# Kernel optimization log

Measured on AMD Instinct MI355X. Metric: run time of the kernel, lower is better.

Reference implementation:

```python
import jax, jax.numpy as jnp
import numpy as np

B, M_CONS, F = 32768, 32, 4
N_ITERS = 400  # fixed-iteration projected-gradient on the dual (Q = I so dual is a box-constrained QP)


def setup_inputs() -> dict:
    key = jax.random.key(0)
    kA, kx, kv, ks = jax.random.split(key, 4)
    A = jax.random.normal(kA, (B, M_CONS, F), dtype=jnp.float32)
    x = jax.random.normal(kx, (B, F), dtype=jnp.float32)
    # Construct b so the polyhedron {w : 2 A w <= b} is nonempty (v0 feasible)
    # with small slacks so many constraints are active (nontrivial QP).
    v0 = jax.random.normal(kv, (B, F), dtype=jnp.float32)
    slack = jnp.abs(jax.random.normal(ks, (B, M_CONS), dtype=jnp.float32)) * 0.1
    b = 2.0 * jnp.einsum('bmf,bf->bm', A, v0) + slack
    return {"A": A, "x": x, "b": b}


def reference(A, x, b):
    # Original: min_z 0.5 z^T Q z + p^T z  s.t. G z <= b, with Q = I (2F x 2F),
    #   G = [A | A]  (cat along feature dim), p = -[x; -x] = [-x; x].
    # Dual (Q = I): min_{lam >= 0} lam^T (G G^T) lam / 1 ... f(lam) = lam^T M lam + q^T lam
    #   with M = 0.5 * 2 * G G^T handled below; z* = -(p + G^T lam*).
    f = x.shape[-1]
    G = jnp.concatenate([A, A], axis=2)            # [B, m, 2F]
    p = jnp.concatenate([-x, x], axis=1)           # [B, 2F]
    M = jnp.einsum('bmi,bni->bmn', G, G)           # [B, m, m] = G G^T
    q = jnp.einsum('bmi,bi->bm', G, p) + b         # [B, m]
    # dual objective: 0.5 lam^T M lam + q^T lam, grad = M lam + q, lam >= 0
    # Lipschitz bound for step size: ||M||_2 <= ||M||_F
    L = jnp.sqrt(jnp.sum(M * M, axis=(1, 2))) + 1e-6   # [B]
    alpha = (1.0 / L)[:, None]                     # [B, 1]
    lam0 = jnp.zeros_like(b)

    def step(lam, _):
        grad = jnp.einsum('bmn,bn->bm', M, lam) + q
        lam = jax.nn.relu(lam - alpha * grad)
        return lam, None

    lam, _ = jax.lax.scan(step, lam0, None, length=N_ITERS)
    z = -(p + jnp.einsum('bmi,bm->bi', G, lam))    # [B, 2F]
    # (y[0:F] + y[F:]) / 2
    return (z[:, :f] + z[:, f:]) * 0.5
```

## Files before the change

### kernel.cpp

```cpp
#include <hip/hip_runtime.h>


#define QP_ITERS 400

typedef float v2f __attribute__((ext_vector_type(2)));

template <int CTRL>
__device__ __forceinline__ float dpp_add(float v) {
    return v + __int_as_float(
        __builtin_amdgcn_update_dpp(0, __float_as_int(v), CTRL, 0xF, 0xF, true));
}

__device__ __forceinline__ float quad_sum(float v) {
    v = dpp_add<0xB1>(v);
    v = dpp_add<0x4E>(v);
    return v;
}

__global__ void __launch_bounds__(256)
__attribute__((amdgpu_waves_per_eu(1, 2)))
qp_pgd_kernel(
        const float* __restrict__ A,
        const float* __restrict__ b,
        float* __restrict__ out,
        int nprob) {
    int t = blockIdx.x * blockDim.x + threadIdx.x;
    int p = t >> 2;
    int j = t & 3;
    if (p >= nprob) return;

    const float4* Ar = reinterpret_cast<const float4*>(A + (size_t)p * 128 + (size_t)j * 32);
    const float4* br = reinterpret_cast<const float4*>(b + (size_t)p * 32 + (size_t)j * 8);

    float ax[8], ay[8], az[8], aw[8];
#pragma unroll
    for (int k = 0; k < 8; ++k) {
        float4 r = Ar[k];
        ax[k] = r.x; ay[k] = r.y; az[k] = r.z; aw[k] = r.w;
    }
    float bb[8];
    {
        float4 b0 = br[0], b1 = br[1];
        bb[0] = b0.x; bb[1] = b0.y; bb[2] = b0.z; bb[3] = b0.w;
        bb[4] = b1.x; bb[5] = b1.y; bb[6] = b1.z; bb[7] = b1.w;
    }

    float s00 = 0.f, s01 = 0.f, s02 = 0.f, s03 = 0.f;
    float s11 = 0.f, s12 = 0.f, s13 = 0.f;
    float s22 = 0.f, s23 = 0.f, s33 = 0.f;
#pragma unroll
    for (int k = 0; k < 8; ++k) {
        s00 = fmaf(ax[k], ax[k], s00);
        s01 = fmaf(ax[k], ay[k], s01);
        s02 = fmaf(ax[k], az[k], s02);
        s03 = fmaf(ax[k], aw[k], s03);
        s11 = fmaf(ay[k], ay[k], s11);
        s12 = fmaf(ay[k], az[k], s12);
        s13 = fmaf(ay[k], aw[k], s13);
        s22 = fmaf(az[k], az[k], s22);
        s23 = fmaf(az[k], aw[k], s23);
        s33 = fmaf(aw[k], aw[k], s33);
    }
    s00 = quad_sum(s00); s01 = quad_sum(s01); s02 = quad_sum(s02); s03 = quad_sum(s03);
    s11 = quad_sum(s11); s12 = quad_sum(s12); s13 = quad_sum(s13);
    s22 = quad_sum(s22); s23 = quad_sum(s23); s33 = quad_sum(s33);
    float ssq = s00 * s00 + s11 * s11 + s22 * s22 + s33 * s33
              + 2.f * (s01 * s01 + s02 * s02 + s03 * s03
                     + s12 * s12 + s13 * s13 + s23 * s23);
    float L = 2.f * sqrtf(ssq) + 1e-6f;
    float alpha = 1.f / L;
    float sc = sqrtf(2.f * alpha);
    float inv_sc = 1.f / sc;

    v2f axp[4], ayp[4], azp[4], awp[4], mcp[4], lamp[4];
#pragma unroll
    for (int i = 0; i < 4; ++i) {
        axp[i] = (v2f){ax[2 * i] * sc, ax[2 * i + 1] * sc};
        ayp[i] = (v2f){ay[2 * i] * sc, ay[2 * i + 1] * sc};
        azp[i] = (v2f){az[2 * i] * sc, az[2 * i + 1] * sc};
        awp[i] = (v2f){aw[2 * i] * sc, aw[2 * i + 1] * sc};
        mcp[i] = (v2f){-alpha * bb[2 * i], -alpha * bb[2 * i + 1]};
        lamp[i] = (v2f){0.f, 0.f};
    }

    for (int it = 0; it < QP_ITERS; ++it) {
        v2f a0 = (v2f){0.f, 0.f}, a1 = (v2f){0.f, 0.f};
        v2f a2 = (v2f){0.f, 0.f}, a3 = (v2f){0.f, 0.f};
#pragma unroll
        for (int i = 0; i < 4; ++i) {
            a0 = __builtin_elementwise_fma(axp[i], lamp[i], a0);
            a1 = __builtin_elementwise_fma(ayp[i], lamp[i], a1);
            a2 = __builtin_elementwise_fma(azp[i], lamp[i], a2);
            a3 = __builtin_elementwise_fma(azp[i], lamp[i], a3);
        }
        a3 = (v2f){0.f, 0.f};
#pragma unroll
        for (int i = 0; i < 4; ++i)
            a3 = __builtin_elementwise_fma(awp[i], lamp[i], a3);

        float u0 = a0.x + a0.y, u1 = a1.x + a1.y;
        float u2 = a2.x + a2.y, u3 = a3.x + a3.y;
        u0 = quad_sum(u0); u1 = quad_sum(u1); u2 = quad_sum(u2); u3 = quad_sum(u3);
        v2f U0 = (v2f){-u0, -u0}, U1 = (v2f){-u1, -u1};
        v2f U2 = (v2f){-u2, -u2}, U3 = (v2f){-u3, -u3};
        const v2f z2 = (v2f){0.f, 0.f};
#pragma unroll
        for (int i = 0; i < 4; ++i) {
            v2f tt = lamp[i] + mcp[i];
            tt = __builtin_elementwise_fma(axp[i], U0, tt);
            tt = __builtin_elementwise_fma(ayp[i], U1, tt);
            tt = __builtin_elementwise_fma(azp[i], U2, tt);
            tt = __builtin_elementwise_fma(awp[i], U3, tt);
            lamp[i] = __builtin_elementwise_max(tt, z2);
        }
    }

    v2f a0 = (v2f){0.f, 0.f}, a1 = (v2f){0.f, 0.f};
    v2f a2 = (v2f){0.f, 0.f}, a3 = (v2f){0.f, 0.f};
#pragma unroll
    for (int i = 0; i < 4; ++i) {
        a0 = __builtin_elementwise_fma(axp[i], lamp[i], a0);
        a1 = __builtin_elementwise_fma(ayp[i], lamp[i], a1);
        a2 = __builtin_elementwise_fma(azp[i], lamp[i], a2);
        a3 = __builtin_elementwise_fma(awp[i], lamp[i], a3);
    }
    float u0 = a0.x + a0.y, u1 = a1.x + a1.y;
    float u2 = a2.x + a2.y, u3 = a3.x + a3.y;
    u0 = quad_sum(u0); u1 = quad_sum(u1); u2 = quad_sum(u2); u3 = quad_sum(u3);
    float r = (j & 1) ? ((j & 2) ? u3 : u1) : ((j & 2) ? u2 : u0);
    out[(size_t)p * 4 + j] = -r * inv_sc;
}

extern "C" void kernel_launch(void* const* d_in, const int* in_sizes, int n_in,
                              void* d_out, int out_size, void* d_ws, size_t ws_size,
                              hipStream_t stream) {
    const float* A = (const float*)d_in[0];
    const float* b = (const float*)d_in[2];
    float* out = (float*)d_out;

    int nprob = in_sizes[2] / 32;
    int threads = nprob * 4;
    dim3 block(256);
    dim3 grid((threads + 255) / 256);
    hipLaunchKernelGGL(qp_pgd_kernel, grid, block, 0, stream, A, b, out, nprob);
}
```

Before: 93.23 us.

## Split each QP across two lanes instead of four to cut shuffle reductions

Each problem is now handled by 2 threads with 16 constraints each instead of 4 threads with 8, so the per-iteration cross-lane reduction needs one DPP step instead of two. It also removes the redundant a3 accumulation over azp, unrolls the iteration loop by 2, tightens waves_per_eu to 1, and writes the output as float2. The cost is fewer total threads (half the waves) and double the per-thread registers, which reduces latency hiding and occupancy.

```diff
diff --git a/kernel.cpp b/kernel.cpp
--- a/kernel.cpp
+++ b/kernel.cpp
@@ -11,45 +11,44 @@
         __builtin_amdgcn_update_dpp(0, __float_as_int(v), CTRL, 0xF, 0xF, true));
 }
 
-__device__ __forceinline__ float quad_sum(float v) {
-    v = dpp_add<0xB1>(v);
-    v = dpp_add<0x4E>(v);
-    return v;
+__device__ __forceinline__ float pair_sum(float v) {
+    return dpp_add<0xB1>(v);
 }
 
 __global__ void __launch_bounds__(256)
-__attribute__((amdgpu_waves_per_eu(1, 2)))
+__attribute__((amdgpu_waves_per_eu(1, 1)))
 qp_pgd_kernel(
         const float* __restrict__ A,
         const float* __restrict__ b,
         float* __restrict__ out,
         int nprob) {
     int t = blockIdx.x * blockDim.x + threadIdx.x;
-    int p = t >> 2;
-    int j = t & 3;
+    int p = t >> 1;
+    int j = t & 1;
     if (p >= nprob) return;
 
-    const float4* Ar = reinterpret_cast<const float4*>(A + (size_t)p * 128 + (size_t)j * 32);
-    const float4* br = reinterpret_cast<const float4*>(b + (size_t)p * 32 + (size_t)j * 8);
+    const float4* Ar = reinterpret_cast<const float4*>(A + (size_t)p * 128 + (size_t)j * 64);
+    const float4* br = reinterpret_cast<const float4*>(b + (size_t)p * 32 + (size_t)j * 16);
 
-    float ax[8], ay[8], az[8], aw[8];
+    float ax[16], ay[16], az[16], aw[16];
 #pragma unroll
-    for (int k = 0; k < 8; ++k) {
+    for (int k = 0; k < 16; ++k) {
         float4 r = Ar[k];
         ax[k] = r.x; ay[k] = r.y; az[k] = r.z; aw[k] = r.w;
     }
-    float bb[8];
-    {
-        float4 b0 = br[0], b1 = br[1];
-        bb[0] = b0.x; bb[1] = b0.y; bb[2] = b0.z; bb[3] = b0.w;
-        bb[4] = b1.x; bb[5] = b1.y; bb[6] = b1.z; bb[7] = b1.w;
+    float bb[16];
+#pragma unroll
+    for (int k = 0; k < 4; ++k) {
+        float4 bv = br[k];
+        bb[4 * k + 0] = bv.x; bb[4 * k + 1] = bv.y;
+        bb[4 * k + 2] = bv.z; bb[4 * k + 3] = bv.w;
     }
 
     float s00 = 0.f, s01 = 0.f, s02 = 0.f, s03 = 0.f;
     float s11 = 0.f, s12 = 0.f, s13 = 0.f;
     float s22 = 0.f, s23 = 0.f, s33 = 0.f;
 #pragma unroll
-    for (int k = 0; k < 8; ++k) {
+    for (int k = 0; k < 16; ++k) {
         s00 = fmaf(ax[k], ax[k], s00);
         s01 = fmaf(ax[k], ay[k], s01);
         s02 = fmaf(ax[k], az[k], s02);
@@ -61,9 +60,9 @@
         s23 = fmaf(az[k], aw[k], s23);
         s33 = fmaf(aw[k], aw[k], s33);
     }
-    s00 = quad_sum(s00); s01 = quad_sum(s01); s02 = quad_sum(s02); s03 = quad_sum(s03);
-    s11 = quad_sum(s11); s12 = quad_sum(s12); s13 = quad_sum(s13);
-    s22 = quad_sum(s22); s23 = quad_sum(s23); s33 = quad_sum(s33);
+    s00 = pair_sum(s00); s01 = pair_sum(s01); s02 = pair_sum(s02); s03 = pair_sum(s03);
+    s11 = pair_sum(s11); s12 = pair_sum(s12); s13 = pair_sum(s13);
+    s22 = pair_sum(s22); s23 = pair_sum(s23); s33 = pair_sum(s33);
     float ssq = s00 * s00 + s11 * s11 + s22 * s22 + s33 * s33
               + 2.f * (s01 * s01 + s02 * s02 + s03 * s03
                      + s12 * s12 + s13 * s13 + s23 * s23);
@@ -72,9 +71,9 @@
     float sc = sqrtf(2.f * alpha);
     float inv_sc = 1.f / sc;
 
-    v2f axp[4], ayp[4], azp[4], awp[4], mcp[4], lamp[4];
+    v2f axp[8], ayp[8], azp[8], awp[8], mcp[8], lamp[8];
 #pragma unroll
-    for (int i = 0; i < 4; ++i) {
+    for (int i = 0; i < 8; ++i) {
         axp[i] = (v2f){ax[2 * i] * sc, ax[2 * i + 1] * sc};
         ayp[i] = (v2f){ay[2 * i] * sc, ay[2 * i + 1] * sc};
         azp[i] = (v2f){az[2 * i] * sc, az[2 * i + 1] * sc};
@@ -83,29 +82,26 @@
         lamp[i] = (v2f){0.f, 0.f};
     }
 
+#pragma unroll 2
     for (int it = 0; it < QP_ITERS; ++it) {
         v2f a0 = (v2f){0.f, 0.f}, a1 = (v2f){0.f, 0.f};
         v2f a2 = (v2f){0.f, 0.f}, a3 = (v2f){0.f, 0.f};
 #pragma unroll
-        for (int i = 0; i < 4; ++i) {
+        for (int i = 0; i < 8; ++i) {
             a0 = __builtin_elementwise_fma(axp[i], lamp[i], a0);
             a1 = __builtin_elementwise_fma(ayp[i], lamp[i], a1);
             a2 = __builtin_elementwise_fma(azp[i], lamp[i], a2);
-            a3 = __builtin_elementwise_fma(azp[i], lamp[i], a3);
+            a3 = __builtin_elementwise_fma(awp[i], lamp[i], a3);
         }
-        a3 = (v2f){0.f, 0.f};
-#pragma unroll
-        for (int i = 0; i < 4; ++i)
-            a3 = __builtin_elementwise_fma(awp[i], lamp[i], a3);
-
-        float u0 = a0.x + a0.y, u1 = a1.x + a1.y;
-        float u2 = a2.x + a2.y, u3 = a3.x + a3.y;
-        u0 = quad_sum(u0); u1 = quad_sum(u1); u2 = quad_sum(u2); u3 = quad_sum(u3);
+        float u0 = pair_sum(a0.x + a0.y);
+        float u1 = pair_sum(a1.x + a1.y);
+        float u2 = pair_sum(a2.x + a2.y);
+        float u3 = pair_sum(a3.x + a3.y);
         v2f U0 = (v2f){-u0, -u0}, U1 = (v2f){-u1, -u1};
         v2f U2 = (v2f){-u2, -u2}, U3 = (v2f){-u3, -u3};
         const v2f z2 = (v2f){0.f, 0.f};
 #pragma unroll
-        for (int i = 0; i < 4; ++i) {
+        for (int i = 0; i < 8; ++i) {
             v2f tt = lamp[i] + mcp[i];
             tt = __builtin_elementwise_fma(axp[i], U0, tt);
             tt = __builtin_elementwise_fma(ayp[i], U1, tt);
@@ -118,17 +114,20 @@
     v2f a0 = (v2f){0.f, 0.f}, a1 = (v2f){0.f, 0.f};
     v2f a2 = (v2f){0.f, 0.f}, a3 = (v2f){0.f, 0.f};
 #pragma unroll
-    for (int i = 0; i < 4; ++i) {
+    for (int i = 0; i < 8; ++i) {
         a0 = __builtin_elementwise_fma(axp[i], lamp[i], a0);
         a1 = __builtin_elementwise_fma(ayp[i], lamp[i], a1);
         a2 = __builtin_elementwise_fma(azp[i], lamp[i], a2);
         a3 = __builtin_elementwise_fma(awp[i], lamp[i], a3);
     }
-    float u0 = a0.x + a0.y, u1 = a1.x + a1.y;
-    float u2 = a2.x + a2.y, u3 = a3.x + a3.y;
-    u0 = quad_sum(u0); u1 = quad_sum(u1); u2 = quad_sum(u2); u3 = quad_sum(u3);
-    float r = (j & 1) ? ((j & 2) ? u3 : u1) : ((j & 2) ? u2 : u0);
-    out[(size_t)p * 4 + j] = -r * inv_sc;
+    float u0 = pair_sum(a0.x + a0.y);
+    float u1 = pair_sum(a1.x + a1.y);
+    float u2 = pair_sum(a2.x + a2.y);
+    float u3 = pair_sum(a3.x + a3.y);
+    float lo = (j == 0) ? u0 : u2;
+    float hi = (j == 0) ? u1 : u3;
+    float2 o = make_float2(-lo * inv_sc, -hi * inv_sc);
+    *reinterpret_cast<float2*>(out + (size_t)p * 4 + (size_t)j * 2) = o;
 }
 
 extern "C" void kernel_launch(void* const* d_in, const int* in_sizes, int n_in,
@@ -139,7 +138,7 @@
     float* out = (float*)d_out;
 
     int nprob = in_sizes[2] / 32;
-    int threads = nprob * 4;
+    int threads = nprob * 2;
     dim3 block(256);
     dim3 grid((threads + 255) / 256);
     hipLaunchKernelGGL(qp_pgd_kernel, grid, block, 0, stream, A, b, out, nprob);
```

Result: faster. 87.38 us, median of 2 (-6.3%).
